# Optimization experiments

Measured on AMD Instinct MI355X. Metric: run time of the kernel, lower is better.

Reference implementation:

```python
import jax, jax.numpy as jnp
import numpy as np

VOCAB, EMBED, HIDDEN, LAYERS = 128, 512, 1024, 2
BATCH, SEQ = 64, 512


def _lstm_layer(x, w_ih, w_hh, b_ih, b_hh):
    # x: [B, T, In]; w_ih: [4H, In]; w_hh: [4H, H]
    B, T, _ = x.shape
    H = w_hh.shape[1]
    # Precompute the input contribution for all timesteps at once: [B, T, 4H]
    xin = jnp.einsum('bti,gi->btg', x, w_ih) + b_ih + b_hh

    def step(carry, xt):
        h, c = carry
        z = xt + h @ w_hh.T                      # [B, 4H]
        i, f, g, o = jnp.split(z, 4, axis=-1)    # PyTorch gate order i,f,g,o
        i = jax.nn.sigmoid(i)
        f = jax.nn.sigmoid(f)
        g = jnp.tanh(g)
        o = jax.nn.sigmoid(o)
        c = f * c + i * g
        h = o * jnp.tanh(c)
        return (h, c), h

    h0 = jnp.zeros((B, H), x.dtype)
    c0 = jnp.zeros((B, H), x.dtype)
    _, hs = jax.lax.scan(step, (h0, c0), jnp.swapaxes(xin, 0, 1))  # [T, B, H]
    return jnp.swapaxes(hs, 0, 1)                                   # [B, T, H]


def setup_inputs() -> dict:
    key = jax.random.key(0)
    ks = jax.random.split(key, 12)
    s_e = 1.0 / np.sqrt(EMBED)
    s_h = 1.0 / np.sqrt(HIDDEN)
    return {
        'x': jax.random.randint(ks[0], (BATCH, SEQ), 0, VOCAB, dtype=jnp.int32),
        'embedding': jax.random.normal(ks[1], (VOCAB, EMBED), jnp.float32),
        'w_ih_0': jax.random.normal(ks[2], (4 * HIDDEN, EMBED), jnp.float32) * s_e,
        'w_hh_0': jax.random.normal(ks[3], (4 * HIDDEN, HIDDEN), jnp.float32) * s_h,
        'b_ih_0': jax.random.normal(ks[4], (4 * HIDDEN,), jnp.float32) * s_h,
        'b_hh_0': jax.random.normal(ks[5], (4 * HIDDEN,), jnp.float32) * s_h,
        'w_ih_1': jax.random.normal(ks[6], (4 * HIDDEN, HIDDEN), jnp.float32) * s_h,
        'w_hh_1': jax.random.normal(ks[7], (4 * HIDDEN, HIDDEN), jnp.float32) * s_h,
        'b_ih_1': jax.random.normal(ks[8], (4 * HIDDEN,), jnp.float32) * s_h,
        'b_hh_1': jax.random.normal(ks[9], (4 * HIDDEN,), jnp.float32) * s_h,
        'fc_w': jax.random.normal(ks[10], (VOCAB, HIDDEN), jnp.float32) * s_h,
        'fc_b': jax.random.normal(ks[11], (VOCAB,), jnp.float32) * s_h,
    }


def reference(x, embedding, w_ih_0, w_hh_0, b_ih_0, b_hh_0,
              w_ih_1, w_hh_1, b_ih_1, b_hh_1, fc_w, fc_b):
    emb = embedding[x]                                   # [B, T, E]
    h1 = _lstm_layer(emb, w_ih_0, w_hh_0, b_ih_0, b_hh_0)  # [B, T, H]
    h2 = _lstm_layer(h1, w_ih_1, w_hh_1, b_ih_1, b_hh_1)   # [B, T, H]
    return h2 @ fc_w.T + fc_b                            # [B, T, V]
```

## Files before the change

### kernel.cpp

```cpp
#include <hip/hip_runtime.h>


typedef _Float16 v8h __attribute__((ext_vector_type(8)));
typedef float v4f __attribute__((ext_vector_type(4)));
typedef _Float16 h2v __attribute__((ext_vector_type(2)));
typedef unsigned long long u64t;

__device__ __forceinline__ float sigf(float x) {
  return 1.0f / (1.0f + __expf(-x));
}
__device__ __forceinline__ float tanhfast(float x) {
  return 1.0f - 2.0f / (1.0f + __expf(2.0f * x));
}

__global__ __launch_bounds__(256) void prep_kernel(
    const float* __restrict__ emb, const float* __restrict__ w_ih0,
    const float* __restrict__ b_ih0, const float* __restrict__ b_hh0,
    const float* __restrict__ fc_w, _Float16* __restrict__ tableV,
    _Float16* __restrict__ fcwT, unsigned* __restrict__ zbuf,
    unsigned* __restrict__ bar) {
  const int blk = blockIdx.x, tid = threadIdx.x;
  if (blk < 2048) {
    const int C = blk * 2 + (tid >> 7);
    const int v = tid & 127;
    const int row =
        ((C >> 2) & 3) * 1024 + (C >> 5) * 8 + ((C >> 4) & 1) * 4 + (C & 3);
    float acc = b_ih0[row] + b_hh0[row];
    const float* er = emb + v * 512;
    const float* wr = w_ih0 + row * 512;
#pragma unroll 4
    for (int k = 0; k < 512; ++k) acc = fmaf(er[k], wr[k], acc);
    tableV[v * 4096 + C] = (_Float16)acc;
  } else if (blk < 2560) {
    const int idx = (blk - 2048) * 256 + tid;
    const int v = idx & 127, k = idx >> 7;
    fcwT[k * 128 + v] = (_Float16)fc_w[v * 1024 + k];
  } else if (blk < 2592) {
    const int idx = (blk - 2560) * 256 + tid;
#pragma unroll
    for (int q = 0; q < 16; ++q) zbuf[idx * 16 + q] = 0u;
  } else {
    for (int i = tid; i < 512; i += 256) bar[i] = 0u;
  }
}

__global__ __launch_bounds__(768, 1) void lstm_mfma(
    const int* __restrict__ x, const _Float16* __restrict__ tableV,
    const float* __restrict__ w_hh0, const float* __restrict__ w_ih1,
    const float* __restrict__ w_hh1, const float* __restrict__ b_ih1,
    const float* __restrict__ b_hh1, _Float16* __restrict__ hseq,
    unsigned* __restrict__ bar) {
  __shared__ __align__(16) float zs[12 * 4 * 8 * 32];

  const int tid = threadIdx.x, blk = blockIdx.x;
  const int w = tid >> 6, l = tid & 63;
  const int lane16 = l & 15, quad = l >> 4;
  const int xcd = blk & 7, bidx = blk >> 3;
  const int m = bidx >> 4, cg = xcd * 16 + (bidx & 15);
  const int kc = (w < 4) ? w : (w - 4);

  v8h breg0[8], breg1[8];
  {
    const int g = lane16 >> 2, j = lane16 & 3;
    const float* Wsrc;
    int kbase;
    if (w < 4) {
      Wsrc = w_hh0;
      kbase = kc * 256;
    } else {
      const int kcomb = kc * 256;
      if (kcomb < 1024) {
        Wsrc = w_ih1;
        kbase = kcomb;
      } else {
        Wsrc = w_hh1;
        kbase = kcomb - 1024;
      }
    }
#pragma unroll
    for (int cb = 0; cb < 2; ++cb) {
      const int row = g * 1024 + cg * 8 + cb * 4 + j;
      const float* rp = Wsrc + row * 1024 + kbase + quad * 8;
#pragma unroll
      for (int kk = 0; kk < 8; ++kk) {
        const float4 f0 = *(const float4*)(rp + kk * 32);
        const float4 f1 = *(const float4*)(rp + kk * 32 + 4);
        v8h b;
        b[0] = (_Float16)f0.x; b[1] = (_Float16)f0.y;
        b[2] = (_Float16)f0.z; b[3] = (_Float16)f0.w;
        b[4] = (_Float16)f1.x; b[5] = (_Float16)f1.y;
        b[6] = (_Float16)f1.z; b[7] = (_Float16)f1.w;
        if (cb == 0) breg0[kk] = b; else breg1[kk] = b;
      }
    }
  }

  const int oj = l & 7, ojj = l & 3, ocb = (l >> 2) & 1;
  const int ob = (w & 3) * 8 + (l >> 3);
  const int obg = m * 32 + ob;
  const int colp = (lane16 & 3) * 4 + (lane16 >> 2);
  const int cswz = colp ^ ((quad & 1) << 4);
  const int rr = ob & 3, rqo = ob >> 2;
  const int rcol = (ocb * 16 + ojj * 4) ^ ((rqo & 1) << 4);

  v4f bias4 = {0.f, 0.f, 0.f, 0.f};
  if (w >= 4 && w < 8) {
#pragma unroll
    for (int g = 0; g < 4; ++g) {
      const int row = g * 1024 + cg * 8 + ocb * 4 + ojj;
      bias4[g] = b_ih1[row] + b_hh1[row];
    }
  }
  _Float16 tvh[4] = {0, 0, 0, 0};
  if (w < 4) {
    const int xv = x[obg * 512];
#pragma unroll
    for (int g = 0; g < 4; ++g)
      tvh[g] = tableV[xv * 4096 + cg * 32 + ocb * 16 + g * 4 + ojj];
  }

  float cst = 0.0f;
  const int gq = blk & 7;

  for (int it = 0; it <= 512; ++it) {
    const _Float16* hr = hseq + (size_t)it * 131072;
    _Float16* hw = hseq + (size_t)(it + 1) * 131072;

    v4f a00 = {0, 0, 0, 0}, a01 = {0, 0, 0, 0};
    v4f a10 = {0, 0, 0, 0}, a11 = {0, 0, 0, 0};
    const bool active = (w < 4) ? (it < 512) : (it >= 1);
    if (active) {
      const _Float16* a0p = hr + (m * 32 + lane16) * 2048 + kc * 256 + quad * 8;
      const _Float16* a1p = a0p + 16 * 2048;
      v8h A0[8], A1[8];
#pragma unroll
      for (int kk = 0; kk < 8; ++kk) A0[kk] = *(const v8h*)(a0p + kk * 32);
#pragma unroll
      for (int kk = 0; kk < 8; ++kk) A1[kk] = *(const v8h*)(a1p + kk * 32);
#pragma unroll
      for (int kk = 0; kk < 8; ++kk) {
        a00 = __builtin_amdgcn_mfma_f32_16x16x32_f16(A0[kk], breg0[kk], a00, 0, 0, 0);
        a10 = __builtin_amdgcn_mfma_f32_16x16x32_f16(A0[kk], breg1[kk], a10, 0, 0, 0);
      }
#pragma unroll
      for (int kk = 0; kk < 8; ++kk) {
        a01 = __builtin_amdgcn_mfma_f32_16x16x32_f16(A1[kk], breg0[kk], a01, 0, 0, 0);
        a11 = __builtin_amdgcn_mfma_f32_16x16x32_f16(A1[kk], breg1[kk], a11, 0, 0, 0);
      }
    }

#pragma unroll
    for (int r = 0; r < 4; ++r) {
      float* zp = &zs[((w * 4 + r) * 8 + quad) * 32];
      zp[cswz] = a00[r];
      zp[128 + cswz] = a01[r];
      zp[cswz ^ 16] = a10[r];
      zp[128 + (cswz ^ 16)] = a11[r];
    }
    __syncthreads();

    const bool do0 = (w < 4) && (it < 512);
    const bool do1 = (w >= 4 && w < 8) && (it >= 1);
    if (do0 || do1) {
      v4f z;
      if (do0) {
        z[0] = (float)tvh[0]; z[1] = (float)tvh[1];
        z[2] = (float)tvh[2]; z[3] = (float)tvh[3];
#pragma unroll
        for (int wv = 0; wv < 4; ++wv)
          z += *(const v4f*)&zs[((wv * 4 + rr) * 8 + rqo) * 32 + rcol];
      } else {
        z = bias4;
#pragma unroll
        for (int wv = 4; wv < 12; ++wv)
          z += *(const v4f*)&zs[((wv * 4 + rr) * 8 + rqo) * 32 + rcol];
      }
      const float ig = sigf(z[0]), fg = sigf(z[1]);
      const float gg = tanhfast(z[2]), og = sigf(z[3]);
      cst = fg * cst + ig * gg;
      const float hv = og * tanhfast(cst);

      const unsigned hu =
          (unsigned)__builtin_bit_cast(unsigned short, (_Float16)hv);
      const unsigned p1 = (unsigned)__shfl_xor((int)hu, 1, 64);
      const unsigned lo = (oj & 1) ? ((p1 & 0xffffu) | (hu << 16))
                                   : ((hu & 0xffffu) | (p1 << 16));
      const unsigned p2 = (unsigned)__shfl_xor((int)lo, 2, 64);
      if ((oj & 3) == 0) {
        const u64t val = (u64t)lo | ((u64t)p2 << 32);
        if (do0) {
          __hip_atomic_store((u64t*)(hw + obg * 2048 + cg * 8 + oj), val,
                             __ATOMIC_RELAXED, __HIP_MEMORY_SCOPE_AGENT);
        } else {
          __hip_atomic_store((u64t*)(hw + obg * 2048 + 1024 + cg * 8 + oj),
                             val, __ATOMIC_RELAXED, __HIP_MEMORY_SCOPE_AGENT);
        }
      }
    }

    if (w < 4 && it + 1 < 512) {
      const int xv = x[obg * 512 + it + 1];
#pragma unroll
      for (int g = 0; g < 4; ++g)
        tvh[g] = tableV[xv * 4096 + cg * 32 + ocb * 16 + g * 4 + ojj];
    }

    if (it < 512) {
      asm volatile("s_waitcnt vmcnt(0)" ::: "memory");
      __syncthreads();
      if (tid == 0) {
        atomicAdd(&bar[(m * 8 + gq) * 16], 1u);
        const unsigned tgt = 16u * (unsigned)(it + 1);
        for (;;) {
          unsigned v[8];
#pragma unroll
          for (int g = 0; g < 8; ++g)
            v[g] = __hip_atomic_load(&bar[(m * 8 + g) * 16], __ATOMIC_RELAXED,
                                     __HIP_MEMORY_SCOPE_AGENT);
          unsigned mn = v[0];
#pragma unroll
          for (int g = 1; g < 8; ++g) mn = (v[g] < mn) ? v[g] : mn;
          if (mn >= tgt) break;
          __builtin_amdgcn_s_sleep(1);
        }
      }
      __syncthreads();
      asm volatile("" ::: "memory");
    }
  }
}

__global__ __launch_bounds__(256, 2) void fc_kernel(
    const _Float16* __restrict__ hseq, const _Float16* __restrict__ fcwT,
    const float* __restrict__ fc_b, float* __restrict__ out) {
  __shared__ float hl[16][1024];
  const int tid = threadIdx.x;
  const int t = blockIdx.x >> 2, bs = blockIdx.x & 3;
  const int v = tid & 127, hh = tid >> 7;

  const h2v* hp = (const h2v*)hseq;
  const size_t base = (size_t)(t + 2) * 65536 + 512;
  for (int idx = tid; idx < 8192; idx += 256) {
    const int bl = idx >> 9, kp = idx & 511;
    const h2v pr = hp[base + (size_t)((bs * 16 + bl)) * 1024 + kp];
    hl[bl][2 * kp] = (float)pr.x;
    hl[bl][2 * kp + 1] = (float)pr.y;
  }
  __syncthreads();

  float acc[8];
#pragma unroll
  for (int i = 0; i < 8; ++i) acc[i] = 0.0f;
  const int bl0 = hh * 8;
#pragma unroll 1
  for (int k4 = 0; k4 < 256; ++k4) {
    const int k = k4 * 4;
    const float w0 = (float)fcwT[(k + 0) * 128 + v];
    const float w1 = (float)fcwT[(k + 1) * 128 + v];
    const float w2 = (float)fcwT[(k + 2) * 128 + v];
    const float w3 = (float)fcwT[(k + 3) * 128 + v];
#pragma unroll
    for (int i = 0; i < 8; ++i) {
      const float4 hv = *(const float4*)&hl[bl0 + i][k];
      acc[i] += hv.x * w0 + hv.y * w1 + hv.z * w2 + hv.w * w3;
    }
  }
  const float bias = fc_b[v];
#pragma unroll
  for (int i = 0; i < 8; ++i) {
    const int bb = bs * 16 + bl0 + i;
    out[(bb * 512 + t) * 128 + v] = acc[i] + bias;
  }
}

extern "C" void kernel_launch(void* const* d_in, const int* in_sizes, int n_in,
                              void* d_out, int out_size, void* d_ws,
                              size_t ws_size, hipStream_t stream) {
  const int* x = (const int*)d_in[0];
  const float* emb = (const float*)d_in[1];
  const float* w_ih0 = (const float*)d_in[2];
  const float* w_hh0 = (const float*)d_in[3];
  const float* b_ih0 = (const float*)d_in[4];
  const float* b_hh0 = (const float*)d_in[5];
  const float* w_ih1 = (const float*)d_in[6];
  const float* w_hh1 = (const float*)d_in[7];
  const float* b_ih1 = (const float*)d_in[8];
  const float* b_hh1 = (const float*)d_in[9];
  const float* fc_w = (const float*)d_in[10];
  const float* fc_b = (const float*)d_in[11];
  float* out = (float*)d_out;

  char* ws = (char*)d_ws;
  _Float16* tableV = (_Float16*)(ws);
  _Float16* fcwT = (_Float16*)(ws + 1048576);
  unsigned* bar = (unsigned*)(ws + 1310720);
  _Float16* hseq = (_Float16*)(ws + 1376256);
  unsigned* zb = (unsigned*)(ws + 1376256);

  prep_kernel<<<2593, 256, 0, stream>>>(emb, w_ih0, b_ih0, b_hh0, fc_w,
                                        tableV, fcwT, zb, bar);

  const _Float16* tableVc = tableV;
  _Float16* hseqa = hseq;
  unsigned* bara = bar;
  void* args[] = {(void*)&x,     (void*)&tableVc, (void*)&w_hh0,
                  (void*)&w_ih1, (void*)&w_hh1,   (void*)&b_ih1,
                  (void*)&b_hh1, (void*)&hseqa,   (void*)&bara};
  hipLaunchCooperativeKernel(lstm_mfma, dim3(256), dim3(768), args, 0, stream);

  fc_kernel<<<2048, 256, 0, stream>>>(hseq, fcwT, fc_b, out);
}
```

Before: 4.880 ms.

## Replace block-wide grid barrier with per-wave fine-grained dataflow counters

```diff
diff --git a/kernel.cpp b/kernel.cpp
--- a/kernel.cpp
+++ b/kernel.cpp
@@ -50,7 +50,8 @@
     const float* __restrict__ w_hh1, const float* __restrict__ b_ih1,
     const float* __restrict__ b_hh1, _Float16* __restrict__ hseq,
     unsigned* __restrict__ bar) {
-  __shared__ __align__(16) float zs[12 * 4 * 8 * 32];
+  __shared__ __align__(16) float zs[2 * 12 * 4 * 8 * 32];
+  const int ZSZ = 12 * 4 * 8 * 32;
 
   const int tid = threadIdx.x, blk = blockIdx.x;
   const int w = tid >> 6, l = tid & 63;
@@ -120,16 +121,25 @@
   }
 
   float cst = 0.0f;
-  const int gq = blk & 7;
+  const unsigned* poll_cp =
+      &bar[(m * 8 + ((w < 8) ? 0 : 4) + (w & 3)) * 16];
+  unsigned* arr_cp = &bar[(m * 8 + ((w < 4) ? 0 : 4) + (cg >> 5)) * 16];
 
   for (int it = 0; it <= 512; ++it) {
     const _Float16* hr = hseq + (size_t)it * 131072;
     _Float16* hw = hseq + (size_t)(it + 1) * 131072;
+    float* zsp = zs + (it & 1) * ZSZ;
 
     v4f a00 = {0, 0, 0, 0}, a01 = {0, 0, 0, 0};
     v4f a10 = {0, 0, 0, 0}, a11 = {0, 0, 0, 0};
     const bool active = (w < 4) ? (it < 512) : (it >= 1);
     if (active) {
+      const unsigned tgt = 128u * (unsigned)((w < 8) ? it : (it - 1));
+      while (__hip_atomic_load(poll_cp, __ATOMIC_RELAXED,
+                               __HIP_MEMORY_SCOPE_AGENT) < tgt)
+        __builtin_amdgcn_s_sleep(1);
+      asm volatile("" ::: "memory");
+
       const _Float16* a0p = hr + (m * 32 + lane16) * 2048 + kc * 256 + quad * 8;
       const _Float16* a1p = a0p + 16 * 2048;
       v8h A0[8], A1[8];
@@ -151,7 +161,7 @@
 
 #pragma unroll
     for (int r = 0; r < 4; ++r) {
-      float* zp = &zs[((w * 4 + r) * 8 + quad) * 32];
+      float* zp = &zsp[((w * 4 + r) * 8 + quad) * 32];
       zp[cswz] = a00[r];
       zp[128 + cswz] = a01[r];
       zp[cswz ^ 16] = a10[r];
@@ -168,12 +178,12 @@
         z[2] = (float)tvh[2]; z[3] = (float)tvh[3];
 #pragma unroll
         for (int wv = 0; wv < 4; ++wv)
-          z += *(const v4f*)&zs[((wv * 4 + rr) * 8 + rqo) * 32 + rcol];
+          z += *(const v4f*)&zsp[((wv * 4 + rr) * 8 + rqo) * 32 + rcol];
       } else {
         z = bias4;
 #pragma unroll
         for (int wv = 4; wv < 12; ++wv)
-          z += *(const v4f*)&zs[((wv * 4 + rr) * 8 + rqo) * 32 + rcol];
+          z += *(const v4f*)&zsp[((wv * 4 + rr) * 8 + rqo) * 32 + rcol];
       }
       const float ig = sigf(z[0]), fg = sigf(z[1]);
       const float gg = tanhfast(z[2]), og = sigf(z[3]);
@@ -196,6 +206,8 @@
                              val, __ATOMIC_RELAXED, __HIP_MEMORY_SCOPE_AGENT);
         }
       }
+      asm volatile("s_waitcnt vmcnt(0)" ::: "memory");
+      if (l == 0) atomicAdd(arr_cp, 1u);
     }
 
     if (w < 4 && it + 1 < 512) {
@@ -203,29 +215,6 @@
 #pragma unroll
       for (int g = 0; g < 4; ++g)
         tvh[g] = tableV[xv * 4096 + cg * 32 + ocb * 16 + g * 4 + ojj];
-    }
-
-    if (it < 512) {
-      asm volatile("s_waitcnt vmcnt(0)" ::: "memory");
-      __syncthreads();
-      if (tid == 0) {
-        atomicAdd(&bar[(m * 8 + gq) * 16], 1u);
-        const unsigned tgt = 16u * (unsigned)(it + 1);
-        for (;;) {
-          unsigned v[8];
-#pragma unroll
-          for (int g = 0; g < 8; ++g)
-            v[g] = __hip_atomic_load(&bar[(m * 8 + g) * 16], __ATOMIC_RELAXED,
-                                     __HIP_MEMORY_SCOPE_AGENT);
-          unsigned mn = v[0];
-#pragma unroll
-          for (int g = 1; g < 8; ++g) mn = (v[g] < mn) ? v[g] : mn;
-          if (mn >= tgt) break;
-          __builtin_amdgcn_s_sleep(1);
-        }
-      }
-      __syncthreads();
-      asm volatile("" ::: "memory");
     }
   }
 }
```

After: 10.55 ms. 116% more time.

## Split LSTM layers across separate block groups with point-to-point wavefront barriers

Applied to the files above, without the earlier changes.

```diff
diff --git a/kernel.cpp b/kernel.cpp
--- a/kernel.cpp
+++ b/kernel.cpp
@@ -25,12 +25,18 @@
     const int v = tid & 127;
     const int row =
         ((C >> 2) & 3) * 1024 + (C >> 5) * 8 + ((C >> 4) & 1) * 4 + (C & 3);
-    float acc = b_ih0[row] + b_hh0[row];
     const float* er = emb + v * 512;
     const float* wr = w_ih0 + row * 512;
+    float a0 = 0.f, a1 = 0.f, a2 = 0.f, a3 = 0.f;
 #pragma unroll 4
-    for (int k = 0; k < 512; ++k) acc = fmaf(er[k], wr[k], acc);
-    tableV[v * 4096 + C] = (_Float16)acc;
+    for (int k = 0; k < 512; k += 4) {
+      a0 = fmaf(er[k], wr[k], a0);
+      a1 = fmaf(er[k + 1], wr[k + 1], a1);
+      a2 = fmaf(er[k + 2], wr[k + 2], a2);
+      a3 = fmaf(er[k + 3], wr[k + 3], a3);
+    }
+    tableV[v * 4096 + C] =
+        (_Float16)(b_ih0[row] + b_hh0[row] + ((a0 + a1) + (a2 + a3)));
   } else if (blk < 2560) {
     const int idx = (blk - 2048) * 256 + tid;
     const int v = idx & 127, k = idx >> 7;
@@ -44,188 +50,246 @@
   }
 }
 
-__global__ __launch_bounds__(768, 1) void lstm_mfma(
+__global__ __launch_bounds__(512, 1) void lstm_mfma(
     const int* __restrict__ x, const _Float16* __restrict__ tableV,
     const float* __restrict__ w_hh0, const float* __restrict__ w_ih1,
     const float* __restrict__ w_hh1, const float* __restrict__ b_ih1,
     const float* __restrict__ b_hh1, _Float16* __restrict__ hseq,
     unsigned* __restrict__ bar) {
-  __shared__ __align__(16) float zs[12 * 4 * 8 * 32];
+  __shared__ __align__(16) float zs[8 * 4 * 8 * 64];
 
   const int tid = threadIdx.x, blk = blockIdx.x;
+  const bool isL1 = blk >= 128;
+  const int sub = isL1 ? blk - 128 : blk;
+  const int xcd = sub & 7, bidx = sub >> 3;
+  const int m = bidx >> 3, cg2 = xcd * 8 + (bidx & 7);
   const int w = tid >> 6, l = tid & 63;
   const int lane16 = l & 15, quad = l >> 4;
-  const int xcd = blk & 7, bidx = blk >> 3;
-  const int m = bidx >> 4, cg = xcd * 16 + (bidx & 15);
-  const int kc = (w < 4) ? w : (w - 4);
-
-  v8h breg0[8], breg1[8];
-  {
-    const int g = lane16 >> 2, j = lane16 & 3;
-    const float* Wsrc;
-    int kbase;
-    if (w < 4) {
-      Wsrc = w_hh0;
-      kbase = kc * 256;
-    } else {
-      const int kcomb = kc * 256;
-      if (kcomb < 1024) {
-        Wsrc = w_ih1;
-        kbase = kcomb;
-      } else {
-        Wsrc = w_hh1;
-        kbase = kcomb - 1024;
-      }
-    }
-#pragma unroll
-    for (int cb = 0; cb < 2; ++cb) {
-      const int row = g * 1024 + cg * 8 + cb * 4 + j;
-      const float* rp = Wsrc + row * 1024 + kbase + quad * 8;
-#pragma unroll
-      for (int kk = 0; kk < 8; ++kk) {
+  const int g = lane16 >> 2, jj = lane16 & 3;
+  const int colp = jj * 4 + g;
+
+  const int b = w * 4 + quad;
+  const int uu = lane16;
+  const int bg = m * 32 + b;
+  const int ubase = (isL1 ? 1024 : 0) + cg2 * 16;
+  const int colo = ((uu >> 2) * 16 + (uu & 3) * 4) ^ ((w & 1) << 4);
+
+  float cst = 0.0f;
+
+  if (!isL1) {
+    v8h bf[4][4];
+#pragma unroll
+    for (int ct = 0; ct < 4; ++ct) {
+      const int row = g * 1024 + cg2 * 16 + ct * 4 + jj;
+      const float* rp = w_hh0 + row * 1024 + w * 128 + quad * 8;
+#pragma unroll
+      for (int kk = 0; kk < 4; ++kk) {
         const float4 f0 = *(const float4*)(rp + kk * 32);
         const float4 f1 = *(const float4*)(rp + kk * 32 + 4);
-        v8h b;
-        b[0] = (_Float16)f0.x; b[1] = (_Float16)f0.y;
-        b[2] = (_Float16)f0.z; b[3] = (_Float16)f0.w;
-        b[4] = (_Float16)f1.x; b[5] = (_Float16)f1.y;
-        b[6] = (_Float16)f1.z; b[7] = (_Float16)f1.w;
-        if (cb == 0) breg0[kk] = b; else breg1[kk] = b;
-      }
-    }
-  }
-
-  const int oj = l & 7, ojj = l & 3, ocb = (l >> 2) & 1;
-  const int ob = (w & 3) * 8 + (l >> 3);
-  const int obg = m * 32 + ob;
-  const int colp = (lane16 & 3) * 4 + (lane16 >> 2);
-  const int cswz = colp ^ ((quad & 1) << 4);
-  const int rr = ob & 3, rqo = ob >> 2;
-  const int rcol = (ocb * 16 + ojj * 4) ^ ((rqo & 1) << 4);
-
-  v4f bias4 = {0.f, 0.f, 0.f, 0.f};
-  if (w >= 4 && w < 8) {
-#pragma unroll
-    for (int g = 0; g < 4; ++g) {
-      const int row = g * 1024 + cg * 8 + ocb * 4 + ojj;
-      bias4[g] = b_ih1[row] + b_hh1[row];
-    }
-  }
-  _Float16 tvh[4] = {0, 0, 0, 0};
-  if (w < 4) {
-    const int xv = x[obg * 512];
-#pragma unroll
-    for (int g = 0; g < 4; ++g)
-      tvh[g] = tableV[xv * 4096 + cg * 32 + ocb * 16 + g * 4 + ojj];
-  }
-
-  float cst = 0.0f;
-  const int gq = blk & 7;
-
-  for (int it = 0; it <= 512; ++it) {
-    const _Float16* hr = hseq + (size_t)it * 131072;
-    _Float16* hw = hseq + (size_t)(it + 1) * 131072;
-
-    v4f a00 = {0, 0, 0, 0}, a01 = {0, 0, 0, 0};
-    v4f a10 = {0, 0, 0, 0}, a11 = {0, 0, 0, 0};
-    const bool active = (w < 4) ? (it < 512) : (it >= 1);
-    if (active) {
-      const _Float16* a0p = hr + (m * 32 + lane16) * 2048 + kc * 256 + quad * 8;
+        v8h bb;
+        bb[0] = (_Float16)f0.x; bb[1] = (_Float16)f0.y;
+        bb[2] = (_Float16)f0.z; bb[3] = (_Float16)f0.w;
+        bb[4] = (_Float16)f1.x; bb[5] = (_Float16)f1.y;
+        bb[6] = (_Float16)f1.z; bb[7] = (_Float16)f1.w;
+        bf[ct][kk] = bb;
+      }
+    }
+    const int Cbase = (cg2 * 2 + (uu >> 3)) * 32 + ((uu >> 2) & 1) * 16 + (uu & 3);
+    _Float16 tvh[4];
+    {
+      const int xv = x[bg * 512];
+#pragma unroll
+      for (int gg = 0; gg < 4; ++gg)
+        tvh[gg] = tableV[xv * 4096 + Cbase + gg * 4];
+    }
+    unsigned* arr = &bar[(m * 8 + xcd) * 16];
+    const unsigned* pw = &bar[(m * 8) * 16];
+
+    for (int it = 0; it < 512; ++it) {
+      if (tid == 0 && it > 0) {
+        const unsigned tgt = 8u * (unsigned)it;
+        for (;;) {
+          unsigned mn = 0xffffffffu;
+#pragma unroll
+          for (int gg = 0; gg < 8; ++gg) {
+            const unsigned vv = __hip_atomic_load(
+                pw + gg * 16, __ATOMIC_RELAXED, __HIP_MEMORY_SCOPE_AGENT);
+            mn = vv < mn ? vv : mn;
+          }
+          if (mn >= tgt) break;
+          __builtin_amdgcn_s_sleep(1);
+        }
+      }
+      __syncthreads();
+      asm volatile("" ::: "memory");
+      const _Float16* hr = hseq + (size_t)it * 131072;
+      _Float16* hw = hseq + (size_t)(it + 1) * 131072;
+
+      const _Float16* a0p = hr + (m * 32 + lane16) * 2048 + w * 128 + quad * 8;
       const _Float16* a1p = a0p + 16 * 2048;
-      v8h A0[8], A1[8];
-#pragma unroll
-      for (int kk = 0; kk < 8; ++kk) A0[kk] = *(const v8h*)(a0p + kk * 32);
-#pragma unroll
-      for (int kk = 0; kk < 8; ++kk) A1[kk] = *(const v8h*)(a1p + kk * 32);
-#pragma unroll
-      for (int kk = 0; kk < 8; ++kk) {
-        a00 = __builtin_amdgcn_mfma_f32_16x16x32_f16(A0[kk], breg0[kk], a00, 0, 0, 0);
-        a10 = __builtin_amdgcn_mfma_f32_16x16x32_f16(A0[kk], breg1[kk], a10, 0, 0, 0);
-      }
-#pragma unroll
-      for (int kk = 0; kk < 8; ++kk) {
-        a01 = __builtin_amdgcn_mfma_f32_16x16x32_f16(A1[kk], breg0[kk], a01, 0, 0, 0);
-        a11 = __builtin_amdgcn_mfma_f32_16x16x32_f16(A1[kk], breg1[kk], a11, 0, 0, 0);
-      }
-    }
-
-#pragma unroll
-    for (int r = 0; r < 4; ++r) {
-      float* zp = &zs[((w * 4 + r) * 8 + quad) * 32];
-      zp[cswz] = a00[r];
-      zp[128 + cswz] = a01[r];
-      zp[cswz ^ 16] = a10[r];
-      zp[128 + (cswz ^ 16)] = a11[r];
-    }
-    __syncthreads();
-
-    const bool do0 = (w < 4) && (it < 512);
-    const bool do1 = (w >= 4 && w < 8) && (it >= 1);
-    if (do0 || do1) {
+      v8h A0[4], A1[4];
+#pragma unroll
+      for (int kk = 0; kk < 4; ++kk) A0[kk] = *(const v8h*)(a0p + kk * 32);
+#pragma unroll
+      for (int kk = 0; kk < 4; ++kk) A1[kk] = *(const v8h*)(a1p + kk * 32);
+      v4f ac0[4] = {{0, 0, 0, 0}, {0, 0, 0, 0}, {0, 0, 0, 0}, {0, 0, 0, 0}};
+      v4f ac1[4] = {{0, 0, 0, 0}, {0, 0, 0, 0}, {0, 0, 0, 0}, {0, 0, 0, 0}};
+#pragma unroll
+      for (int kk = 0; kk < 4; ++kk)
+#pragma unroll
+        for (int ct = 0; ct < 4; ++ct) {
+          ac0[ct] = __builtin_amdgcn_mfma_f32_16x16x32_f16(A0[kk], bf[ct][kk], ac0[ct], 0, 0, 0);
+          ac1[ct] = __builtin_amdgcn_mfma_f32_16x16x32_f16(A1[kk], bf[ct][kk], ac1[ct], 0, 0, 0);
+        }
+
+#pragma unroll
+      for (int r = 0; r < 4; ++r)
+#pragma unroll
+        for (int ct = 0; ct < 4; ++ct) {
+          const int col = (ct * 16 + colp) ^ ((quad & 1) << 4);
+          zs[((w * 4 + r) * 8 + quad) * 64 + col] = ac0[ct][r];
+          zs[((w * 4 + r) * 8 + 4 + quad) * 64 + col] = ac1[ct][r];
+        }
+      __syncthreads();
+
       v4f z;
-      if (do0) {
-        z[0] = (float)tvh[0]; z[1] = (float)tvh[1];
-        z[2] = (float)tvh[2]; z[3] = (float)tvh[3];
-#pragma unroll
-        for (int wv = 0; wv < 4; ++wv)
-          z += *(const v4f*)&zs[((wv * 4 + rr) * 8 + rqo) * 32 + rcol];
-      } else {
-        z = bias4;
-#pragma unroll
-        for (int wv = 4; wv < 12; ++wv)
-          z += *(const v4f*)&zs[((wv * 4 + rr) * 8 + rqo) * 32 + rcol];
-      }
+      z[0] = (float)tvh[0]; z[1] = (float)tvh[1];
+      z[2] = (float)tvh[2]; z[3] = (float)tvh[3];
+#pragma unroll
+      for (int wv = 0; wv < 8; ++wv)
+        z += *(const v4f*)&zs[((wv * 4 + quad) * 8 + w) * 64 + colo];
       const float ig = sigf(z[0]), fg = sigf(z[1]);
-      const float gg = tanhfast(z[2]), og = sigf(z[3]);
-      cst = fg * cst + ig * gg;
+      const float gg2 = tanhfast(z[2]), og = sigf(z[3]);
+      cst = fg * cst + ig * gg2;
       const float hv = og * tanhfast(cst);
 
       const unsigned hu =
           (unsigned)__builtin_bit_cast(unsigned short, (_Float16)hv);
       const unsigned p1 = (unsigned)__shfl_xor((int)hu, 1, 64);
-      const unsigned lo = (oj & 1) ? ((p1 & 0xffffu) | (hu << 16))
-                                   : ((hu & 0xffffu) | (p1 << 16));
+      const unsigned lo = (l & 1) ? ((p1 & 0xffffu) | (hu << 16))
+                                  : ((hu & 0xffffu) | (p1 << 16));
       const unsigned p2 = (unsigned)__shfl_xor((int)lo, 2, 64);
-      if ((oj & 3) == 0) {
+      if ((l & 3) == 0) {
         const u64t val = (u64t)lo | ((u64t)p2 << 32);
-        if (do0) {
-          __hip_atomic_store((u64t*)(hw + obg * 2048 + cg * 8 + oj), val,
-                             __ATOMIC_RELAXED, __HIP_MEMORY_SCOPE_AGENT);
-        } else {
-          __hip_atomic_store((u64t*)(hw + obg * 2048 + 1024 + cg * 8 + oj),
-                             val, __ATOMIC_RELAXED, __HIP_MEMORY_SCOPE_AGENT);
-        }
-      }
-    }
-
-    if (w < 4 && it + 1 < 512) {
-      const int xv = x[obg * 512 + it + 1];
-#pragma unroll
-      for (int g = 0; g < 4; ++g)
-        tvh[g] = tableV[xv * 4096 + cg * 32 + ocb * 16 + g * 4 + ojj];
-    }
-
-    if (it < 512) {
+        __hip_atomic_store((u64t*)(hw + bg * 2048 + ubase + (l & 15)), val,
+                           __ATOMIC_RELAXED, __HIP_MEMORY_SCOPE_AGENT);
+      }
+      if (it + 1 < 512) {
+        const int xv = x[bg * 512 + it + 1];
+#pragma unroll
+        for (int gg = 0; gg < 4; ++gg)
+          tvh[gg] = tableV[xv * 4096 + Cbase + gg * 4];
+      }
       asm volatile("s_waitcnt vmcnt(0)" ::: "memory");
       __syncthreads();
+      if (tid == 0) atomicAdd(arr, 1u);
+    }
+  } else {
+    v8h bf[4][8];
+    {
+      const float* Wsrc = (w < 4) ? w_ih1 : w_hh1;
+      const int kbase = (w < 4) ? w * 256 : w * 256 - 1024;
+#pragma unroll
+      for (int ct = 0; ct < 4; ++ct) {
+        const int row = g * 1024 + cg2 * 16 + ct * 4 + jj;
+        const float* rp = Wsrc + row * 1024 + kbase + quad * 8;
+#pragma unroll
+        for (int kk = 0; kk < 8; ++kk) {
+          const float4 f0 = *(const float4*)(rp + kk * 32);
+          const float4 f1 = *(const float4*)(rp + kk * 32 + 4);
+          v8h bb;
+          bb[0] = (_Float16)f0.x; bb[1] = (_Float16)f0.y;
+          bb[2] = (_Float16)f0.z; bb[3] = (_Float16)f0.w;
+          bb[4] = (_Float16)f1.x; bb[5] = (_Float16)f1.y;
+          bb[6] = (_Float16)f1.z; bb[7] = (_Float16)f1.w;
+          bf[ct][kk] = bb;
+        }
+      }
+    }
+    v4f bias4;
+#pragma unroll
+    for (int gg = 0; gg < 4; ++gg) {
+      const int row = gg * 1024 + cg2 * 16 + uu;
+      bias4[gg] = b_ih1[row] + b_hh1[row];
+    }
+    unsigned* arr = &bar[((2 + m) * 8 + xcd) * 16];
+    const unsigned* pw0 = &bar[(m * 8) * 16];
+    const unsigned* pw1 = &bar[((2 + m) * 8) * 16];
+
+    for (int it = 1; it <= 512; ++it) {
       if (tid == 0) {
-        atomicAdd(&bar[(m * 8 + gq) * 16], 1u);
-        const unsigned tgt = 16u * (unsigned)(it + 1);
+        const unsigned t0 = 8u * (unsigned)it;
+        const unsigned t1 = 8u * (unsigned)(it - 1);
         for (;;) {
-          unsigned v[8];
-#pragma unroll
-          for (int g = 0; g < 8; ++g)
-            v[g] = __hip_atomic_load(&bar[(m * 8 + g) * 16], __ATOMIC_RELAXED,
-                                     __HIP_MEMORY_SCOPE_AGENT);
-          unsigned mn = v[0];
-#pragma unroll
-          for (int g = 1; g < 8; ++g) mn = (v[g] < mn) ? v[g] : mn;
-          if (mn >= tgt) break;
+          unsigned mn0 = 0xffffffffu, mn1 = 0xffffffffu;
+#pragma unroll
+          for (int gg = 0; gg < 8; ++gg) {
+            const unsigned v0 = __hip_atomic_load(
+                pw0 + gg * 16, __ATOMIC_RELAXED, __HIP_MEMORY_SCOPE_AGENT);
+            const unsigned v1 = __hip_atomic_load(
+                pw1 + gg * 16, __ATOMIC_RELAXED, __HIP_MEMORY_SCOPE_AGENT);
+            mn0 = v0 < mn0 ? v0 : mn0;
+            mn1 = v1 < mn1 ? v1 : mn1;
+          }
+          if (mn0 >= t0 && mn1 >= t1) break;
           __builtin_amdgcn_s_sleep(1);
         }
       }
       __syncthreads();
       asm volatile("" ::: "memory");
+      const _Float16* hr = hseq + (size_t)it * 131072;
+      _Float16* hw = hseq + (size_t)(it + 1) * 131072;
+
+      const _Float16* a0p = hr + (m * 32 + lane16) * 2048 + w * 256 + quad * 8;
+      const _Float16* a1p = a0p + 16 * 2048;
+      v8h A0[8], A1[8];
+#pragma unroll
+      for (int kk = 0; kk < 8; ++kk) A0[kk] = *(const v8h*)(a0p + kk * 32);
+#pragma unroll
+      for (int kk = 0; kk < 8; ++kk) A1[kk] = *(const v8h*)(a1p + kk * 32);
+      v4f ac0[4] = {{0, 0, 0, 0}, {0, 0, 0, 0}, {0, 0, 0, 0}, {0, 0, 0, 0}};
+      v4f ac1[4] = {{0, 0, 0, 0}, {0, 0, 0, 0}, {0, 0, 0, 0}, {0, 0, 0, 0}};
+#pragma unroll
+      for (int kk = 0; kk < 8; ++kk)
+#pragma unroll
+        for (int ct = 0; ct < 4; ++ct) {
+          ac0[ct] = __builtin_amdgcn_mfma_f32_16x16x32_f16(A0[kk], bf[ct][kk], ac0[ct], 0, 0, 0);
+          ac1[ct] = __builtin_amdgcn_mfma_f32_16x16x32_f16(A1[kk], bf[ct][kk], ac1[ct], 0, 0, 0);
+        }
+
+#pragma unroll
+      for (int r = 0; r < 4; ++r)
+#pragma unroll
+        for (int ct = 0; ct < 4; ++ct) {
+          const int col = (ct * 16 + colp) ^ ((quad & 1) << 4);
+          zs[((w * 4 + r) * 8 + quad) * 64 + col] = ac0[ct][r];
+          zs[((w * 4 + r) * 8 + 4 + quad) * 64 + col] = ac1[ct][r];
+        }
+      __syncthreads();
+
+      v4f z = bias4;
+#pragma unroll
+      for (int wv = 0; wv < 8; ++wv)
+        z += *(const v4f*)&zs[((wv * 4 + quad) * 8 + w) * 64 + colo];
+      const float ig = sigf(z[0]), fg = sigf(z[1]);
+      const float gg2 = tanhfast(z[2]), og = sigf(z[3]);
+      cst = fg * cst + ig * gg2;
+      const float hv = og * tanhfast(cst);
+
+      const unsigned hu =
+          (unsigned)__builtin_bit_cast(unsigned short, (_Float16)hv);
+      const unsigned p1 = (unsigned)__shfl_xor((int)hu, 1, 64);
+      const unsigned lo = (l & 1) ? ((p1 & 0xffffu) | (hu << 16))
+                                  : ((hu & 0xffffu) | (p1 << 16));
+      const unsigned p2 = (unsigned)__shfl_xor((int)lo, 2, 64);
+      if ((l & 3) == 0) {
+        const u64t val = (u64t)lo | ((u64t)p2 << 32);
+        __hip_atomic_store((u64t*)(hw + bg * 2048 + ubase + (l & 15)), val,
+                           __ATOMIC_RELAXED, __HIP_MEMORY_SCOPE_AGENT);
+      }
+      asm volatile("s_waitcnt vmcnt(0)" ::: "memory");
+      __syncthreads();
+      if (tid == 0) atomicAdd(arr, 1u);
     }
   }
 }
@@ -306,7 +370,7 @@
   void* args[] = {(void*)&x,     (void*)&tableVc, (void*)&w_hh0,
                   (void*)&w_ih1, (void*)&w_hh1,   (void*)&b_ih1,
                   (void*)&b_hh1, (void*)&hseqa,   (void*)&bara};
-  hipLaunchCooperativeKernel(lstm_mfma, dim3(256), dim3(768), args, 0, stream);
+  hipLaunchCooperativeKernel(lstm_mfma, dim3(256), dim3(512), args, 0, stream);
 
   fc_kernel<<<2048, 256, 0, stream>>>(hseq, fcwT, fc_b, out);
 }
```

New measurement: 3.967 ms. -18.7%, faster.
